# Kernel tuning notes

Measured on AMD Instinct MI355X. Metric: run time of the kernel, lower is better.

## Reference

```python
import jax, jax.numpy as jnp
import numpy as np

DIM = 1024
NUM_HEADS = 16
HEAD_DIM = DIM // NUM_HEADS


def setup_inputs() -> dict:
    key = jax.random.key(0)
    ks = jax.random.split(key, 5)
    scale = 1.0 / np.sqrt(DIM)
    return {
        "x": jax.random.normal(ks[0], (2, 2048, DIM), dtype=jnp.float32),
        "qkv_w": jax.random.normal(ks[1], (3 * DIM, DIM), dtype=jnp.float32) * scale,
        "qkv_b": jax.random.normal(ks[2], (3 * DIM,), dtype=jnp.float32) * 0.01,
        "proj_w": jax.random.normal(ks[3], (DIM, DIM), dtype=jnp.float32) * scale,
        "proj_b": jax.random.normal(ks[4], (DIM,), dtype=jnp.float32) * 0.01,
    }


def reference(x, qkv_w, qkv_b, proj_w, proj_b):
    B, N, D = x.shape
    H, Hd = NUM_HEADS, HEAD_DIM
    # fused QKV projection: [B,N,3D]
    qkv = jnp.einsum('bnd,ed->bne', x, qkv_w) + qkv_b
    qkv = qkv.reshape(B, N, 3, H, Hd)
    q = qkv[:, :, 0].transpose(0, 2, 1, 3)  # [B,H,N,Hd]
    k = qkv[:, :, 1].transpose(0, 2, 1, 3)
    v = qkv[:, :, 2].transpose(0, 2, 1, 3)
    scale = 1.0 / jnp.sqrt(jnp.asarray(Hd, dtype=x.dtype))
    scores = jnp.einsum('bhqd,bhkd->bhqk', q, k) * scale  # [B,H,N,N]
    attn = jax.nn.softmax(scores, axis=-1)
    out = jnp.einsum('bhqk,bhkd->bhqd', attn, v)  # [B,H,N,Hd]
    out = out.transpose(0, 2, 1, 3).reshape(B, N, D)
    return jnp.einsum('bnd,ed->bne', out, proj_w) + proj_b
```

## Files before the change

kernel.cpp:

```cpp
#include <hip/hip_runtime.h>
#include <hip/hip_bf16.h>
#include <stdint.h>


typedef __bf16 bf16;
typedef __bf16 bf16x2 __attribute__((ext_vector_type(2)));
typedef __bf16 bf16x4 __attribute__((ext_vector_type(4)));
typedef __bf16 bf16x8 __attribute__((ext_vector_type(8)));
typedef float  f32x4  __attribute__((ext_vector_type(4)));
typedef float  f32x16 __attribute__((ext_vector_type(16)));
typedef uint32_t u32x4 __attribute__((ext_vector_type(4)));

#define QSCALE 0.18033688011112042f

__device__ __forceinline__ void gload_lds16(const void* g, void* l) {
    __builtin_amdgcn_global_load_lds(
        (const __attribute__((address_space(1))) void*)(uintptr_t)g,
        (__attribute__((address_space(3))) void*)(uint32_t)(uintptr_t)l,
        16, 0, 0);
}

__device__ __forceinline__ uint32_t pkbf(float a, float b) {
    bf16x2 t = { (bf16)a, (bf16)b };
    return __builtin_bit_cast(uint32_t, t);
}

__global__ void cast_all(const float* __restrict__ x,
                         const float* __restrict__ qw,
                         const float* __restrict__ pw,
                         bf16* __restrict__ xb, bf16* __restrict__ wq,
                         bf16* __restrict__ wp) {
    int i = blockIdx.x * blockDim.x + threadIdx.x;
    const float4* src; bf16x4* dst; int off;
    if (i < 1048576)      { src = (const float4*)x;  dst = (bf16x4*)xb; off = i; }
    else if (i < 1835008) { src = (const float4*)qw; dst = (bf16x4*)wq; off = i - 1048576; }
    else                  { src = (const float4*)pw; dst = (bf16x4*)wp; off = i - 1835008; }
    float4 v = src[off];
    bf16x4 o = { (bf16)v.x, (bf16)v.y, (bf16)v.z, (bf16)v.w };
    dst[off] = o;
}

template<int EPI>
__global__ __launch_bounds__(256) void gemm128(
    const bf16* __restrict__ A,
    const bf16* __restrict__ Bw,
    const float* __restrict__ bias,
    float* __restrict__ outF,
    bf16* __restrict__ qb, bf16* __restrict__ kf, bf16* __restrict__ vf,
    int K)
{
    __shared__ __align__(16) char gsm[EPI == 0 ? 36864 : 32768];
    bf16* ct = (bf16*)gsm;
    const int tid  = threadIdx.x;
    const int lane = tid & 63, w = tid >> 6;
    const int g = lane >> 4, lr = lane & 15;
    const int wr = w >> 1, wc = w & 1;
    int mt, nt;
    if (EPI == 0) {
        int bid = blockIdx.x;
        int xcd = bid & 7, i = bid >> 3;
        mt = xcd * 4 + i / 24;
        nt = i % 24;
    } else {
        nt = blockIdx.x; mt = blockIdx.y;
    }
    const int mbase = mt * 128, nbase = nt * 128;

    f32x4 acc[4][4] = {};

    auto stg = [&](int buf, int it) {
        const bf16* Ag = A  + (size_t)mbase * K + it * 32;
        const bf16* Bg = Bw + (size_t)nbase * K + it * 32;
        bf16* as = (bf16*)(gsm + buf * 16384);
        bf16* bs = (bf16*)(gsm + buf * 16384 + 8192);
        int c0 = tid, c1 = 256 + tid;
        gload_lds16(Ag + (size_t)(c0 >> 2) * K + (c0 & 3) * 8, as + c0 * 8);
        gload_lds16(Bg + (size_t)(c0 >> 2) * K + (c0 & 3) * 8, bs + c0 * 8);
        gload_lds16(Ag + (size_t)(c1 >> 2) * K + (c1 & 3) * 8, as + c1 * 8);
        gload_lds16(Bg + (size_t)(c1 >> 2) * K + (c1 & 3) * 8, bs + c1 * 8);
    };

    const int nIt = K >> 5;
    stg(0, 0);
    __syncthreads();

    #pragma unroll 2
    for (int it = 0; it < nIt; ++it) {
        const int cur = it & 1;
        if (it + 1 < nIt) stg(cur ^ 1, it + 1);

        const bf16* as = (const bf16*)(gsm + cur * 16384);
        const bf16* bs = as + 4096;
        bf16x8 af[4], bfr[4];
        #pragma unroll
        for (int mi = 0; mi < 4; ++mi)
            af[mi] = *(const bf16x8*)(as + (wr * 64 + mi * 16 + lr) * 32 + g * 8);
        #pragma unroll
        for (int ni = 0; ni < 4; ++ni)
            bfr[ni] = *(const bf16x8*)(bs + (wc * 64 + ni * 16 + lr) * 32 + g * 8);
        #pragma unroll
        for (int mi = 0; mi < 4; ++mi)
            #pragma unroll
            for (int ni = 0; ni < 4; ++ni)
                acc[mi][ni] = __builtin_amdgcn_mfma_f32_16x16x32_bf16(
                    af[mi], bfr[ni], acc[mi][ni], 0, 0, 0);

        __syncthreads();
    }

    if (EPI == 1) {
        #pragma unroll
        for (int ni = 0; ni < 4; ++ni) {
            int e = nbase + wc * 64 + ni * 16 + lr;
            float bv = bias[e];
            #pragma unroll
            for (int mi = 0; mi < 4; ++mi) {
                #pragma unroll
                for (int r = 0; r < 4; ++r) {
                    int token = mbase + wr * 64 + mi * 16 + g * 4 + r;
                    outF[(size_t)token * 1024 + e] = acc[mi][ni][r] + bv;
                }
            }
        }
    } else {
        const int sec = nbase >> 10;
        #pragma unroll
        for (int ni = 0; ni < 4; ++ni) {
            int ec = wc * 64 + ni * 16 + lr;
            float bv = bias[nbase + ec];
            #pragma unroll
            for (int mi = 0; mi < 4; ++mi) {
                #pragma unroll
                for (int r = 0; r < 4; ++r) {
                    int tl = wr * 64 + mi * 16 + g * 4 + r;
                    float v = acc[mi][ni][r] + bv;
                    if (sec == 0) v *= QSCALE;
                    int row = (sec == 2) ? ec : tl;
                    int col = (sec == 2) ? tl : ec;
                    ct[row * 144 + col] = (bf16)v;
                }
            }
        }
        __syncthreads();
        const int b  = mbase >> 11;
        const int h0 = (nbase & 1023) >> 6;
        const int mb = mbase & 2047;
        #pragma unroll
        for (int si = 0; si < 8; ++si) {
            int c   = si * 256 + tid;
            int hh  = c >> 10;
            int w10 = c & 1023;
            int bh  = b * 16 + h0 + hh;
            int lrow, lcol;
            size_t gaddr;
            bf16* dst;
            if (sec == 0) {
                int nl = w10 >> 3, d0 = (w10 & 7) * 8;
                lrow = nl; lcol = hh * 64 + d0;
                gaddr = ((size_t)bh * 2048 + mb + nl) * 64 + d0;
                dst = qb;
            } else if (sec == 1) {
                int o = w10 * 8;
                int frag = o >> 9, l = (o >> 3) & 63;
                int nl = (frag >> 2) * 32 + (l & 31);
                int d0 = (frag & 3) * 16 + (l >> 5) * 8;
                lrow = nl; lcol = hh * 64 + d0;
                gaddr = ((size_t)(bh * 64 + (mb >> 5))) * 2048 + o;
                dst = kf;
            } else {
                int o = w10 * 8;
                int n6 = o >> 12, r2 = o & 4095;
                int d5 = r2 >> 11, r3 = r2 & 2047;
                int nc = r3 >> 9,  l  = (r3 >> 3) & 63;
                int d  = d5 * 32 + (l & 31);
                int n0 = n6 * 64 + nc * 16 + (l >> 5) * 8;
                lrow = hh * 64 + d; lcol = n0;
                gaddr = ((size_t)(bh * 32 + (mb >> 6))) * 4096 + o;
                dst = vf;
            }
            *(bf16x8*)(dst + gaddr) = *(const bf16x8*)(&ct[lrow * 144 + lcol]);
        }
    }
}

__global__ __launch_bounds__(512, 2) void attn32(
    const bf16* __restrict__ Q,
    const bf16* __restrict__ Kf,
    const bf16* __restrict__ Vf,
    bf16* __restrict__ Ao,
    int Nseq)
{
    __shared__ __align__(16) char smem[65536];
    bf16*  KsB = (bf16*)smem;
    bf16*  VsB = (bf16*)(smem + 32768);
    float* xch = (float*)smem;
    bf16*  otp = (bf16*)(smem + 36864);

    const int tid  = threadIdx.x;
    const int lane = tid & 63;
    const int u    = tid >> 6;
    const int half = u >> 2, qw = u & 3;
    const int hi = lane >> 5, ql = lane & 31;
    const int bid = blockIdx.x;
    const int xcd = bid & 7, ii = bid >> 3;
    const int bh = xcd * 4 + (ii >> 3), qc = ii & 7;
    const int h = bh & 15, b = bh >> 4;
    const int q0 = qc * 256 + qw * 64;

    const bf16* Qh  = Q  + (size_t)bh * Nseq * 64;
    const bf16* Kfh = Kf + (size_t)bh * Nseq * 64;
    const bf16* Vfh = Vf + (size_t)bh * Nseq * 64;

    bf16x8 qfA[4], qfB[4];
    #pragma unroll
    for (int c = 0; c < 4; ++c) {
        qfA[c] = *(const bf16x8*)(Qh + (size_t)(q0 + ql) * 64 + c * 16 + hi * 8);
        qfB[c] = *(const bf16x8*)(Qh + (size_t)(q0 + 32 + ql) * 64 + c * 16 + hi * 8);
    }

    bf16x8 vones;
    #pragma unroll
    for (int i = 0; i < 8; ++i) vones[i] = (bf16)1.0f;

    f32x16 o0A = {}, o1A = {}, laA = {};
    f32x16 o0B = {}, o1B = {}, laB = {};

    const int nch = (Nseq >> 6) >> 1;
    const int hk  = half * nch;

    auto stage = [&](int buf, int t) {
        const bf16* Kc = Kfh + (size_t)(hk + t) * 4096;
        const bf16* Vc = Vfh + (size_t)(hk + t) * 4096;
        bf16* kd = KsB + (half * 2 + buf) * 4096;
        bf16* vd = VsB + (half * 2 + buf) * 4096;
        int ht = tid & 255;
        gload_lds16(Kc + ht * 8,        kd + ht * 8);
        gload_lds16(Kc + 2048 + ht * 8, kd + 2048 + ht * 8);
        gload_lds16(Vc + ht * 8,        vd + ht * 8);
        gload_lds16(Vc + 2048 + ht * 8, vd + 2048 + ht * 8);
    };

    stage(0, 0);
    __syncthreads();

    #pragma unroll 2
    for (int t = 0; t < nch; ++t) {
        const int cur = t & 1;
        if (t + 1 < nch) stage(cur ^ 1, t + 1);

        const bf16* kl = KsB + (half * 2 + cur) * 4096;
        const bf16* vl = VsB + (half * 2 + cur) * 4096;
        bf16x8 kin[8], vfr[8];
        #pragma unroll
        for (int i = 0; i < 8; ++i)
            kin[i] = *(const bf16x8*)(kl + i * 512 + lane * 8);
        #pragma unroll
        for (int i = 0; i < 8; ++i)
            vfr[i] = *(const bf16x8*)(vl + i * 512 + lane * 8);

        {
            f32x16 s0 = {}, s1 = {};
            #pragma unroll
            for (int c = 0; c < 4; ++c) {
                s0 = __builtin_amdgcn_mfma_f32_32x32x16_bf16(kin[c],     qfA[c], s0, 0, 0, 0);
                s1 = __builtin_amdgcn_mfma_f32_32x32x16_bf16(kin[4 + c], qfA[c], s1, 0, 0, 0);
            }
            float p0[16], p1[16];
            #pragma unroll
            for (int r = 0; r < 16; ++r) { p0[r] = __builtin_amdgcn_exp2f(s0[r]); }
            #pragma unroll
            for (int r = 0; r < 16; ++r) { p1[r] = __builtin_amdgcn_exp2f(s1[r]); }
            bf16x8 pfr[4];
            #pragma unroll
            for (int f = 0; f < 4; ++f) {
                const float* pp = (f < 2) ? p0 : p1;
                const int base = (f & 1) * 8;
                union { uint32_t u[4]; bf16x8 v; } pw;
                #pragma unroll
                for (int wd = 0; wd < 2; ++wd) {
                    uint32_t X = pkbf(pp[base + 2*wd], pp[base + 2*wd + 1]);
                    uint32_t Y = pkbf(pp[base + 4 + 2*wd], pp[base + 4 + 2*wd + 1]);
                    auto rr = __builtin_amdgcn_permlane32_swap((int)X, (int)Y, false, false);
                    pw.u[wd]     = (uint32_t)rr[0];
                    pw.u[2 + wd] = (uint32_t)rr[1];
                }
                pfr[f] = pw.v;
            }
            #pragma unroll
            for (int f = 0; f < 4; ++f) {
                o0A = __builtin_amdgcn_mfma_f32_32x32x16_bf16(vfr[f],     pfr[f], o0A, 0, 0, 0);
                o1A = __builtin_amdgcn_mfma_f32_32x32x16_bf16(vfr[4 + f], pfr[f], o1A, 0, 0, 0);
                laA = __builtin_amdgcn_mfma_f32_32x32x16_bf16(vones,      pfr[f], laA, 0, 0, 0);
            }
        }
        {
            f32x16 s0 = {}, s1 = {};
            #pragma unroll
            for (int c = 0; c < 4; ++c) {
                s0 = __builtin_amdgcn_mfma_f32_32x32x16_bf16(kin[c],     qfB[c], s0, 0, 0, 0);
                s1 = __builtin_amdgcn_mfma_f32_32x32x16_bf16(kin[4 + c], qfB[c], s1, 0, 0, 0);
            }
            float p0[16], p1[16];
            #pragma unroll
            for (int r = 0; r < 16; ++r) { p0[r] = __builtin_amdgcn_exp2f(s0[r]); }
            #pragma unroll
            for (int r = 0; r < 16; ++r) { p1[r] = __builtin_amdgcn_exp2f(s1[r]); }
            bf16x8 pfr[4];
            #pragma unroll
            for (int f = 0; f < 4; ++f) {
                const float* pp = (f < 2) ? p0 : p1;
                const int base = (f & 1) * 8;
                union { uint32_t u[4]; bf16x8 v; } pw;
                #pragma unroll
                for (int wd = 0; wd < 2; ++wd) {
                    uint32_t X = pkbf(pp[base + 2*wd], pp[base + 2*wd + 1]);
                    uint32_t Y = pkbf(pp[base + 4 + 2*wd], pp[base + 4 + 2*wd + 1]);
                    auto rr = __builtin_amdgcn_permlane32_swap((int)X, (int)Y, false, false);
                    pw.u[wd]     = (uint32_t)rr[0];
                    pw.u[2 + wd] = (uint32_t)rr[1];
                }
                pfr[f] = pw.v;
            }
            #pragma unroll
            for (int f = 0; f < 4; ++f) {
                o0B = __builtin_amdgcn_mfma_f32_32x32x16_bf16(vfr[f],     pfr[f], o0B, 0, 0, 0);
                o1B = __builtin_amdgcn_mfma_f32_32x32x16_bf16(vfr[4 + f], pfr[f], o1B, 0, 0, 0);
                laB = __builtin_amdgcn_mfma_f32_32x32x16_bf16(vones,      pfr[f], laB, 0, 0, 0);
            }
        }

        __syncthreads();
    }

    auto finish = [&](const f32x16& po0, const f32x16& po1, const f32x16& pla, int qp) {
        float lsum = pla[0];
        __syncthreads();
        if (half == 1) {
            float* xp = xch + ((size_t)(qw * 64 + lane)) * 36;
            *(f32x16*)(xp)      = po0;
            *(f32x16*)(xp + 16) = po1;
            xp[32] = lsum;
        }
        __syncthreads();
        if (half == 0) {
            const float* xp = xch + ((size_t)(qw * 64 + lane)) * 36;
            f32x16 oa = *(const f32x16*)(xp);
            f32x16 ob = *(const f32x16*)(xp + 16);
            f32x16 m0 = po0 + oa;
            f32x16 m1 = po1 + ob;
            float ls = lsum + xp[32];
            float linv = __builtin_amdgcn_rcpf(ls);
            #pragma unroll
            for (int qd = 0; qd < 4; ++qd) {
                int dbase = 8 * qd + 4 * hi;
                bf16* orow = otp + (qw * 32 + ql) * 66;
                *(uint32_t*)(orow + dbase)          = pkbf(m0[4*qd] * linv,   m0[4*qd+1] * linv);
                *(uint32_t*)(orow + dbase + 2)      = pkbf(m0[4*qd+2] * linv, m0[4*qd+3] * linv);
                *(uint32_t*)(orow + 32 + dbase)     = pkbf(m1[4*qd] * linv,   m1[4*qd+1] * linv);
                *(uint32_t*)(orow + 32 + dbase + 2) = pkbf(m1[4*qd+2] * linv, m1[4*qd+3] * linv);
            }
            __asm__ volatile("s_waitcnt lgkmcnt(0)" ::: "memory");
            const int t = lane >> 1, e = lane & 1;
            uint32_t rw[16];
            #pragma unroll
            for (int j = 0; j < 16; ++j)
                rw[j] = *(const uint32_t*)(otp + (qw * 32 + t) * 66 + e * 32 + 2 * j);
            size_t gbase = (size_t)(b * Nseq + q0 + qp + t) * 1024 + h * 64 + e * 32;
            #pragma unroll
            for (int v = 0; v < 4; ++v) {
                u32x4 sv = { rw[4*v], rw[4*v+1], rw[4*v+2], rw[4*v+3] };
                *(u32x4*)(Ao + gbase + v * 8) = sv;
            }
        }
    };
    finish(o0A, o1A, laA, 0);
    finish(o0B, o1B, laB, 32);
}

extern "C" void kernel_launch(void* const* d_in, const int* in_sizes, int n_in,
                              void* d_out, int out_size, void* d_ws, size_t ws_size,
                              hipStream_t stream) {
    const float* x      = (const float*)d_in[0];
    const float* qkv_w  = (const float*)d_in[1];
    const float* qkv_b  = (const float*)d_in[2];
    const float* proj_w = (const float*)d_in[3];
    const float* proj_b = (const float*)d_in[4];
    float* out = (float*)d_out;

    char* ws = (char*)d_ws;
    bf16* xb    = (bf16*)(ws);
    bf16* wqkv  = (bf16*)(ws + ((size_t)8  << 20));
    bf16* wproj = (bf16*)(ws + ((size_t)14 << 20));
    bf16* qb    = (bf16*)(ws + ((size_t)16 << 20));
    bf16* kf    = (bf16*)(ws + ((size_t)24 << 20));
    bf16* vf    = (bf16*)(ws + ((size_t)32 << 20));
    bf16* att   = (bf16*)(ws);

    cast_all<<<dim3(8192), dim3(256), 0, stream>>>(x, qkv_w, proj_w, xb, wqkv, wproj);

    gemm128<0><<<dim3(768), dim3(256), 0, stream>>>(
        xb, wqkv, qkv_b, (float*)nullptr, qb, kf, vf, 1024);

    attn32<<<dim3(256), dim3(512), 0, stream>>>(qb, kf, vf, att, 2048);

    gemm128<1><<<dim3(8, 32), dim3(256), 0, stream>>>(
        att, wproj, proj_b, out, (bf16*)nullptr, (bf16*)nullptr, (bf16*)nullptr, 1024);
}
```

Baseline: 106.8 us.

## Fuse fp32-to-bf16 casts into GEMM operand staging and drop cast kernel

Removes the separate cast kernel that converted x and both weight matrices to bf16. The GEMMs now load fp32 operands into registers, convert and pack them to bf16, and write them to LDS after the MFMA work of each iteration, so conversion overlaps with compute. This saves a launch and the extra write and read of the bf16 copies. In exchange each GEMM reads twice the bytes per operand, and weight tiles are re-converted by every block that uses them, which adds VALU work and register pressure.

Result: slower. 115.6 us (+8.3%).

```diff
diff --git a/kernel.cpp b/kernel.cpp
--- a/kernel.cpp
+++ b/kernel.cpp
@@ -5,7 +5,6 @@
 
 typedef __bf16 bf16;
 typedef __bf16 bf16x2 __attribute__((ext_vector_type(2)));
-typedef __bf16 bf16x4 __attribute__((ext_vector_type(4)));
 typedef __bf16 bf16x8 __attribute__((ext_vector_type(8)));
 typedef float  f32x4  __attribute__((ext_vector_type(4)));
 typedef float  f32x16 __attribute__((ext_vector_type(16)));
@@ -25,25 +24,20 @@
     return __builtin_bit_cast(uint32_t, t);
 }
 
-__global__ void cast_all(const float* __restrict__ x,
-                         const float* __restrict__ qw,
-                         const float* __restrict__ pw,
-                         bf16* __restrict__ xb, bf16* __restrict__ wq,
-                         bf16* __restrict__ wp) {
-    int i = blockIdx.x * blockDim.x + threadIdx.x;
-    const float4* src; bf16x4* dst; int off;
-    if (i < 1048576)      { src = (const float4*)x;  dst = (bf16x4*)xb; off = i; }
-    else if (i < 1835008) { src = (const float4*)qw; dst = (bf16x4*)wq; off = i - 1048576; }
-    else                  { src = (const float4*)pw; dst = (bf16x4*)wp; off = i - 1835008; }
-    float4 v = src[off];
-    bf16x4 o = { (bf16)v.x, (bf16)v.y, (bf16)v.z, (bf16)v.w };
-    dst[off] = o;
+__device__ __forceinline__ bf16x8 pk8(const f32x4& a, const f32x4& b) {
+    union { uint32_t u[4]; bf16x8 v; } r;
+    r.u[0] = pkbf(a[0], a[1]);
+    r.u[1] = pkbf(a[2], a[3]);
+    r.u[2] = pkbf(b[0], b[1]);
+    r.u[3] = pkbf(b[2], b[3]);
+    return r.v;
 }
 
 template<int EPI>
 __global__ __launch_bounds__(256) void gemm128(
-    const bf16* __restrict__ A,
-    const bf16* __restrict__ Bw,
+    const float* __restrict__ Af,
+    const bf16*  __restrict__ Ab,
+    const float* __restrict__ Bwf,
     const float* __restrict__ bias,
     float* __restrict__ outF,
     bf16* __restrict__ qb, bf16* __restrict__ kf, bf16* __restrict__ vf,
@@ -54,7 +48,7 @@
     const int tid  = threadIdx.x;
     const int lane = tid & 63, w = tid >> 6;
     const int g = lane >> 4, lr = lane & 15;
-    const int wr = w >> 1, wc = w & 1;
+    const int wr2 = w >> 1, wc = w & 1;
     int mt, nt;
     if (EPI == 0) {
         int bid = blockIdx.x;
@@ -68,33 +62,62 @@
 
     f32x4 acc[4][4] = {};
 
-    auto stg = [&](int buf, int it) {
-        const bf16* Ag = A  + (size_t)mbase * K + it * 32;
-        const bf16* Bg = Bw + (size_t)nbase * K + it * 32;
+    const int r0 = tid >> 2, k0 = (tid & 3) * 8;
+    const int r1 = r0 + 64;
+    f32x4 tA[4], tB[4];
+
+    auto ldA = [&](int it) {
+        const float* Ag = Af + (size_t)mbase * K + it * 32;
+        tA[0] = *(const f32x4*)(Ag + (size_t)r0 * K + k0);
+        tA[1] = *(const f32x4*)(Ag + (size_t)r0 * K + k0 + 4);
+        tA[2] = *(const f32x4*)(Ag + (size_t)r1 * K + k0);
+        tA[3] = *(const f32x4*)(Ag + (size_t)r1 * K + k0 + 4);
+    };
+    auto ldAlds = [&](int buf, int it) {
+        const bf16* Ag = Ab + (size_t)mbase * K + it * 32;
         bf16* as = (bf16*)(gsm + buf * 16384);
-        bf16* bs = (bf16*)(gsm + buf * 16384 + 8192);
-        int c0 = tid, c1 = 256 + tid;
-        gload_lds16(Ag + (size_t)(c0 >> 2) * K + (c0 & 3) * 8, as + c0 * 8);
-        gload_lds16(Bg + (size_t)(c0 >> 2) * K + (c0 & 3) * 8, bs + c0 * 8);
-        gload_lds16(Ag + (size_t)(c1 >> 2) * K + (c1 & 3) * 8, as + c1 * 8);
-        gload_lds16(Bg + (size_t)(c1 >> 2) * K + (c1 & 3) * 8, bs + c1 * 8);
+        gload_lds16(Ag + (size_t)r0 * K + k0, as + tid * 8);
+        gload_lds16(Ag + (size_t)r1 * K + k0, as + (256 + tid) * 8);
+    };
+    auto ldB = [&](int it) {
+        const float* Bg = Bwf + (size_t)nbase * K + it * 32;
+        tB[0] = *(const f32x4*)(Bg + (size_t)r0 * K + k0);
+        tB[1] = *(const f32x4*)(Bg + (size_t)r0 * K + k0 + 4);
+        tB[2] = *(const f32x4*)(Bg + (size_t)r1 * K + k0);
+        tB[3] = *(const f32x4*)(Bg + (size_t)r1 * K + k0 + 4);
+    };
+    auto wrstg = [&](int buf) {
+        bf16* as = (bf16*)(gsm + buf * 16384);
+        bf16* bs = as + 4096;
+        if (EPI == 0) {
+            *(bf16x8*)(as + tid * 8)         = pk8(tA[0], tA[1]);
+            *(bf16x8*)(as + (256 + tid) * 8) = pk8(tA[2], tA[3]);
+        }
+        *(bf16x8*)(bs + tid * 8)         = pk8(tB[0], tB[1]);
+        *(bf16x8*)(bs + (256 + tid) * 8) = pk8(tB[2], tB[3]);
     };
 
     const int nIt = K >> 5;
-    stg(0, 0);
+    if (EPI == 0) ldA(0); else ldAlds(0, 0);
+    ldB(0);
+    wrstg(0);
     __syncthreads();
 
     #pragma unroll 2
     for (int it = 0; it < nIt; ++it) {
         const int cur = it & 1;
-        if (it + 1 < nIt) stg(cur ^ 1, it + 1);
+        const bool pf = (it + 1 < nIt);
+        if (pf) {
+            if (EPI == 0) ldA(it + 1); else ldAlds(cur ^ 1, it + 1);
+            ldB(it + 1);
+        }
 
         const bf16* as = (const bf16*)(gsm + cur * 16384);
         const bf16* bs = as + 4096;
         bf16x8 af[4], bfr[4];
         #pragma unroll
         for (int mi = 0; mi < 4; ++mi)
-            af[mi] = *(const bf16x8*)(as + (wr * 64 + mi * 16 + lr) * 32 + g * 8);
+            af[mi] = *(const bf16x8*)(as + (wr2 * 64 + mi * 16 + lr) * 32 + g * 8);
         #pragma unroll
         for (int ni = 0; ni < 4; ++ni)
             bfr[ni] = *(const bf16x8*)(bs + (wc * 64 + ni * 16 + lr) * 32 + g * 8);
@@ -105,6 +128,7 @@
                 acc[mi][ni] = __builtin_amdgcn_mfma_f32_16x16x32_bf16(
                     af[mi], bfr[ni], acc[mi][ni], 0, 0, 0);
 
+        if (pf) wrstg(cur ^ 1);
         __syncthreads();
     }
 
@@ -117,7 +141,7 @@
             for (int mi = 0; mi < 4; ++mi) {
                 #pragma unroll
                 for (int r = 0; r < 4; ++r) {
-                    int token = mbase + wr * 64 + mi * 16 + g * 4 + r;
+                    int token = mbase + wr2 * 64 + mi * 16 + g * 4 + r;
                     outF[(size_t)token * 1024 + e] = acc[mi][ni][r] + bv;
                 }
             }
@@ -132,7 +156,7 @@
             for (int mi = 0; mi < 4; ++mi) {
                 #pragma unroll
                 for (int r = 0; r < 4; ++r) {
-                    int tl = wr * 64 + mi * 16 + g * 4 + r;
+                    int tl = wr2 * 64 + mi * 16 + g * 4 + r;
                     float v = acc[mi][ni][r] + bv;
                     if (sec == 0) v *= QSCALE;
                     int row = (sec == 2) ? ec : tl;
@@ -388,21 +412,17 @@
     float* out = (float*)d_out;
 
     char* ws = (char*)d_ws;
-    bf16* xb    = (bf16*)(ws);
-    bf16* wqkv  = (bf16*)(ws + ((size_t)8  << 20));
-    bf16* wproj = (bf16*)(ws + ((size_t)14 << 20));
     bf16* qb    = (bf16*)(ws + ((size_t)16 << 20));
     bf16* kf    = (bf16*)(ws + ((size_t)24 << 20));
     bf16* vf    = (bf16*)(ws + ((size_t)32 << 20));
     bf16* att   = (bf16*)(ws);
 
-    cast_all<<<dim3(8192), dim3(256), 0, stream>>>(x, qkv_w, proj_w, xb, wqkv, wproj);
-
     gemm128<0><<<dim3(768), dim3(256), 0, stream>>>(
-        xb, wqkv, qkv_b, (float*)nullptr, qb, kf, vf, 1024);
+        x, (const bf16*)nullptr, qkv_w, qkv_b, (float*)nullptr, qb, kf, vf, 1024);
 
     attn32<<<dim3(256), dim3(512), 0, stream>>>(qb, kf, vf, att, 2048);
 
     gemm128<1><<<dim3(8, 32), dim3(256), 0, stream>>>(
-        att, wproj, proj_b, out, (bf16*)nullptr, (bf16*)nullptr, (bf16*)nullptr, 1024);
-}
+        (const float*)nullptr, att, proj_w, proj_b, out,
+        (bf16*)nullptr, (bf16*)nullptr, (bf16*)nullptr, 1024);
+}
```
